# Kernel optimization log

Measured on AMD Instinct MI355X. Metric: run time of the kernel, lower is better.

## Reference

```python
import jax, jax.numpy as jnp
import numpy as np

EPI_AGE_PENALTY = 0.02
EPI_MIN_STRENGTH = 0.001
EPI_STRENGTH_BOOST = 0.5
RMS_EPS = 1e-6


def setup_inputs() -> dict:
    key = jax.random.key(0)
    k1, k2, k3, k4, k5, k6 = jax.random.split(key, 6)
    B, S, D = 32, 8192, 512
    return {
        "q_win": jax.random.normal(k1, (B, D), dtype=jnp.float32),
        "epi_keys": jax.random.normal(k2, (B, S, D), dtype=jnp.float32),
        "epi_vals": jax.random.normal(k3, (B, S, D), dtype=jnp.float32),
        "epi_age": jax.random.uniform(k4, (B, S), dtype=jnp.float32),
        "epi_strength": jax.random.uniform(k5, (B, S), dtype=jnp.float32),
        "scale": jnp.ones((D,), dtype=jnp.float32),  # RMSNorm learned scale
    }


def reference(q_win, epi_keys, epi_vals, epi_age, epi_strength, scale):
    # L2-normalize query [B,D] and keys [B,S,D]
    qn = q_win / (jnp.linalg.norm(q_win, axis=-1, keepdims=True) + 1e-6)
    kn = epi_keys / (jnp.linalg.norm(epi_keys, axis=-1, keepdims=True) + 1e-6)
    # cosine similarity [B,S]
    sim = jnp.einsum("bsd,bd->bs", kn, qn)
    str_log = jnp.log(jnp.clip(epi_strength, EPI_MIN_STRENGTH, 1e9))
    logits = sim + EPI_STRENGTH_BOOST * str_log - EPI_AGE_PENALTY * epi_age
    alive = (epi_strength > EPI_MIN_STRENGTH).astype(jnp.float32)
    logits = logits + (alive - 1.0) * 1000.0
    w = jax.nn.softmax(logits, axis=-1)
    # softmax-weighted read over slots -> [B,D]
    read = jnp.einsum("bs,bsd->bd", w, epi_vals)
    # RMSNorm
    rms = jnp.sqrt(jnp.mean(jnp.square(read), axis=-1, keepdims=True) + RMS_EPS)
    read = read / rms * scale
    return (read, w, logits)
```

## Files before the change

### kernel.cpp

```cpp
#include <hip/hip_runtime.h>
#include <math.h>

#define BB 32
#define SS 8192
#define DD 512
#define D4 (DD / 4)
#define CHUNKS 64
#define CHUNK 128

static constexpr float AGE_PEN = 0.02f;
static constexpr float MIN_STR = 0.001f;
static constexpr float STR_BOOST = 0.5f;
static constexpr float RMS_EPS_F = 1e-6f;

__device__ inline float dot4(float4 a, float4 b) {
    return a.x * b.x + a.y * b.y + a.z * b.z + a.w * b.w;
}

__device__ inline float block_sum(float v, volatile float* red) {
    int tid = threadIdx.x, lane = tid & 63, wid = tid >> 6;
#pragma unroll
    for (int off = 32; off; off >>= 1) v += __shfl_xor(v, off);
    if (lane == 0) red[wid] = v;
    __syncthreads();
    float r = red[0] + red[1] + red[2] + red[3];
    __syncthreads();
    return r;
}

__global__ __launch_bounds__(256) void fused_kernel(
    const float4* __restrict__ keys, const float4* __restrict__ vals,
    const float* __restrict__ q, const float* __restrict__ age,
    const float* __restrict__ strength, float* __restrict__ logits,
    float4* __restrict__ partial, float* __restrict__ esum_partial) {
    __shared__ float4 racc[4 * D4];
    __shared__ float e_sh[CHUNK];
    __shared__ float rede[4];

    int chunk = blockIdx.x, b = blockIdx.y;
    int tid = threadIdx.x, wid = tid >> 6, lane = tid & 63;

    const float4* q4 = (const float4*)q + b * D4;
    float4 q0 = q4[lane], q1 = q4[lane + 64];
    float qq = dot4(q0, q0) + dot4(q1, q1);
#pragma unroll
    for (int off = 32; off; off >>= 1) qq += __shfl_xor(qq, off);
    float qinv = 1.f / (sqrtf(qq) + 1e-6f);
    q0.x *= qinv; q0.y *= qinv; q0.z *= qinv; q0.w *= qinv;
    q1.x *= qinv; q1.y *= qinv; q1.z *= qinv; q1.w *= qinv;

    long long s0 = (long long)b * SS + chunk * CHUNK;

    float esum = 0.f;
#pragma unroll 2
    for (int s = wid; s < CHUNK; s += 4) {
        long long row = s0 + s;
        const float4* k = keys + row * D4;
        float4 k0 = k[lane], k1 = k[lane + 64];

        float kk = dot4(k0, k0) + dot4(k1, k1);
        float kq = dot4(k0, q0) + dot4(k1, q1);
#pragma unroll
        for (int off = 32; off; off >>= 1) {
            kk += __shfl_xor(kk, off);
            kq += __shfl_xor(kq, off);
        }
        float st = strength[row];
        float a = age[row];
        float lg = kq / (sqrtf(kk) + 1e-6f)
                 + STR_BOOST * logf(fminf(fmaxf(st, MIN_STR), 1e9f))
                 - AGE_PEN * a;
        if (!(st > MIN_STR)) lg -= 1000.f;
        float e = expf(lg);
        esum += e;
        if (lane == 0) {
            logits[row] = lg;
            e_sh[s] = e;
        }
    }
    if (lane == 0) rede[wid] = esum;
    __syncthreads();

    float4 acc0 = {0.f, 0.f, 0.f, 0.f}, acc1 = {0.f, 0.f, 0.f, 0.f};
#pragma unroll 4
    for (int s = wid; s < CHUNK; s += 4) {
        long long row = s0 + s;
        const float4* v = vals + row * D4;
        float e = e_sh[s];
        float4 v0 = v[lane], v1 = v[lane + 64];
        acc0.x += e * v0.x; acc0.y += e * v0.y; acc0.z += e * v0.z; acc0.w += e * v0.w;
        acc1.x += e * v1.x; acc1.y += e * v1.y; acc1.z += e * v1.z; acc1.w += e * v1.w;
    }

    racc[wid * D4 + lane] = acc0;
    racc[wid * D4 + 64 + lane] = acc1;
    __syncthreads();

    if (tid < D4) {
        float4 a0 = racc[tid], a1 = racc[D4 + tid], a2 = racc[2 * D4 + tid], a3 = racc[3 * D4 + tid];
        float4 r;
        r.x = a0.x + a1.x + a2.x + a3.x;
        r.y = a0.y + a1.y + a2.y + a3.y;
        r.z = a0.z + a1.z + a2.z + a3.z;
        r.w = a0.w + a1.w + a2.w + a3.w;
        partial[((long long)b * CHUNKS + chunk) * D4 + tid] = r;
    } else if (tid == D4) {
        esum_partial[b * CHUNKS + chunk] = rede[0] + rede[1] + rede[2] + rede[3];
    }
}

__global__ __launch_bounds__(256) void reduce_rms_kernel(
    const float* __restrict__ partial, const float* __restrict__ esum_partial,
    const float* __restrict__ scale, float* __restrict__ readout,
    float* __restrict__ inv_esum) {
    __shared__ float red[4];
    int b = blockIdx.x, tid = threadIdx.x;

    const float* p = partial + (long long)b * CHUNKS * DD;
    float r0 = 0.f, r1 = 0.f;
#pragma unroll 4
    for (int c = 0; c < CHUNKS; c++) {
        r0 += p[c * DD + tid];
        r1 += p[c * DD + tid + 256];
    }
    float le = (tid < CHUNKS) ? esum_partial[b * CHUNKS + tid] : 0.f;
    float etot = block_sum(le, red);
    float inv_e = 1.f / etot;
    if (tid == 0) inv_esum[b] = inv_e;
    r0 *= inv_e;
    r1 *= inv_e;
    float ss = block_sum(r0 * r0 + r1 * r1, red);
    float rms = sqrtf(ss / (float)DD + RMS_EPS_F);
    float inv = 1.f / rms;
    readout[b * DD + tid] = r0 * inv * scale[tid];
    readout[b * DD + tid + 256] = r1 * inv * scale[tid + 256];
}

__global__ __launch_bounds__(256) void w_kernel(const float4* __restrict__ logits,
                                                const float* __restrict__ inv_esum,
                                                float4* __restrict__ w) {
    int i4 = blockIdx.x * 256 + threadIdx.x;
    int b = i4 >> 11;
    float inv = inv_esum[b];
    float4 lg = logits[i4];
    float4 r;
    r.x = expf(lg.x) * inv;
    r.y = expf(lg.y) * inv;
    r.z = expf(lg.z) * inv;
    r.w = expf(lg.w) * inv;
    w[i4] = r;
}

extern "C" void kernel_launch(void* const* d_in, const int* in_sizes, int n_in,
                              void* d_out, int out_size, void* d_ws, size_t ws_size,
                              hipStream_t stream) {
    const float* q        = (const float*)d_in[0];
    const float* keys     = (const float*)d_in[1];
    const float* vals     = (const float*)d_in[2];
    const float* age      = (const float*)d_in[3];
    const float* strength = (const float*)d_in[4];
    const float* scale    = (const float*)d_in[5];

    float* out = (float*)d_out;
    float* readout = out;
    float* w       = out + BB * DD;
    float* logits  = out + BB * DD + BB * SS;

    float* ws = (float*)d_ws;
    float* partial      = ws;
    float* esum_partial = ws + BB * CHUNKS * DD;
    float* inv_esum     = esum_partial + BB * CHUNKS;

    fused_kernel<<<dim3(CHUNKS, BB), 256, 0, stream>>>(
        (const float4*)keys, (const float4*)vals, q, age, strength,
        logits, (float4*)partial, esum_partial);
    reduce_rms_kernel<<<BB, 256, 0, stream>>>(partial, esum_partial, scale, readout, inv_esum);
    w_kernel<<<BB * SS / 4 / 256, 256, 0, stream>>>((const float4*)logits, inv_esum, (float4*)w);
}
```

Measured before the change: 206.7 us.

## Split fused kernel into per-row logits kernel and separate weighted-sum kernel

```diff
diff --git a/kernel.cpp b/kernel.cpp
--- a/kernel.cpp
+++ b/kernel.cpp
@@ -28,17 +28,13 @@
     return r;
 }
 
-__global__ __launch_bounds__(256) void fused_kernel(
-    const float4* __restrict__ keys, const float4* __restrict__ vals,
-    const float* __restrict__ q, const float* __restrict__ age,
-    const float* __restrict__ strength, float* __restrict__ logits,
-    float4* __restrict__ partial, float* __restrict__ esum_partial) {
-    __shared__ float4 racc[4 * D4];
-    __shared__ float e_sh[CHUNK];
-    __shared__ float rede[4];
-
-    int chunk = blockIdx.x, b = blockIdx.y;
-    int tid = threadIdx.x, wid = tid >> 6, lane = tid & 63;
+__global__ __launch_bounds__(256) void logits_e_kernel(
+    const float4* __restrict__ keys, const float* __restrict__ q,
+    const float* __restrict__ age, const float* __restrict__ strength,
+    float* __restrict__ logits, float* __restrict__ e_out) {
+    int wid = threadIdx.x >> 6, lane = threadIdx.x & 63;
+    int row = blockIdx.x * 4 + wid;
+    int b = row >> 13;
 
     const float4* q4 = (const float4*)q + b * D4;
     float4 q0 = q4[lane], q1 = q4[lane + 64];
@@ -46,67 +42,57 @@
 #pragma unroll
     for (int off = 32; off; off >>= 1) qq += __shfl_xor(qq, off);
     float qinv = 1.f / (sqrtf(qq) + 1e-6f);
-    q0.x *= qinv; q0.y *= qinv; q0.z *= qinv; q0.w *= qinv;
-    q1.x *= qinv; q1.y *= qinv; q1.z *= qinv; q1.w *= qinv;
 
-    long long s0 = (long long)b * SS + chunk * CHUNK;
-
-    float esum = 0.f;
-#pragma unroll 2
-    for (int s = wid; s < CHUNK; s += 4) {
-        long long row = s0 + s;
-        const float4* k = keys + row * D4;
-        float4 k0 = k[lane], k1 = k[lane + 64];
-
-        float kk = dot4(k0, k0) + dot4(k1, k1);
-        float kq = dot4(k0, q0) + dot4(k1, q1);
+    const float4* k = keys + (long long)row * D4;
+    float4 k0 = k[lane], k1 = k[lane + 64];
+    float kk = dot4(k0, k0) + dot4(k1, k1);
+    float kq = dot4(k0, q0) + dot4(k1, q1);
 #pragma unroll
-        for (int off = 32; off; off >>= 1) {
-            kk += __shfl_xor(kk, off);
-            kq += __shfl_xor(kq, off);
-        }
+    for (int off = 32; off; off >>= 1) {
+        kk += __shfl_xor(kk, off);
+        kq += __shfl_xor(kq, off);
+    }
+    if (lane == 0) {
         float st = strength[row];
         float a = age[row];
-        float lg = kq / (sqrtf(kk) + 1e-6f)
-                 + STR_BOOST * logf(fminf(fmaxf(st, MIN_STR), 1e9f))
-                 - AGE_PEN * a;
+        float sim = kq * qinv / (sqrtf(kk) + 1e-6f);
+        float lg = sim + STR_BOOST * logf(fminf(fmaxf(st, MIN_STR), 1e9f)) - AGE_PEN * a;
         if (!(st > MIN_STR)) lg -= 1000.f;
-        float e = expf(lg);
-        esum += e;
-        if (lane == 0) {
-            logits[row] = lg;
-            e_sh[s] = e;
-        }
+        logits[row] = lg;
+        e_out[row] = expf(lg);
     }
-    if (lane == 0) rede[wid] = esum;
+}
+
+__global__ __launch_bounds__(128) void wsum_kernel(
+    const float4* __restrict__ vals, const float* __restrict__ e,
+    float4* __restrict__ partial, float* __restrict__ esum_partial) {
+    __shared__ float sw[CHUNK];
+    __shared__ float rede[2];
+    int chunk = blockIdx.x, b = blockIdx.y, tid = threadIdx.x;
+    int s0 = chunk * CHUNK;
+    float my_e = e[b * SS + s0 + tid];
+    sw[tid] = my_e;
     __syncthreads();
 
-    float4 acc0 = {0.f, 0.f, 0.f, 0.f}, acc1 = {0.f, 0.f, 0.f, 0.f};
+    const float4* vbase = vals + ((long long)b * SS + s0) * D4 + tid;
+    float4 acc = {0.f, 0.f, 0.f, 0.f};
 #pragma unroll 4
-    for (int s = wid; s < CHUNK; s += 4) {
-        long long row = s0 + s;
-        const float4* v = vals + row * D4;
-        float e = e_sh[s];
-        float4 v0 = v[lane], v1 = v[lane + 64];
-        acc0.x += e * v0.x; acc0.y += e * v0.y; acc0.z += e * v0.z; acc0.w += e * v0.w;
-        acc1.x += e * v1.x; acc1.y += e * v1.y; acc1.z += e * v1.z; acc1.w += e * v1.w;
+    for (int s = 0; s < CHUNK; s++) {
+        float4 v = vbase[(long long)s * D4];
+        float ww = sw[s];
+        acc.x += ww * v.x;
+        acc.y += ww * v.y;
+        acc.z += ww * v.z;
+        acc.w += ww * v.w;
     }
+    partial[((long long)b * CHUNKS + chunk) * D4 + tid] = acc;
 
-    racc[wid * D4 + lane] = acc0;
-    racc[wid * D4 + 64 + lane] = acc1;
+    float t = my_e;
+#pragma unroll
+    for (int off = 32; off; off >>= 1) t += __shfl_xor(t, off);
+    if ((tid & 63) == 0) rede[tid >> 6] = t;
     __syncthreads();
-
-    if (tid < D4) {
-        float4 a0 = racc[tid], a1 = racc[D4 + tid], a2 = racc[2 * D4 + tid], a3 = racc[3 * D4 + tid];
-        float4 r;
-        r.x = a0.x + a1.x + a2.x + a3.x;
-        r.y = a0.y + a1.y + a2.y + a3.y;
-        r.z = a0.z + a1.z + a2.z + a3.z;
-        r.w = a0.w + a1.w + a2.w + a3.w;
-        partial[((long long)b * CHUNKS + chunk) * D4 + tid] = r;
-    } else if (tid == D4) {
-        esum_partial[b * CHUNKS + chunk] = rede[0] + rede[1] + rede[2] + rede[3];
-    }
+    if (tid == 0) esum_partial[b * CHUNKS + chunk] = rede[0] + rede[1];
 }
 
 __global__ __launch_bounds__(256) void reduce_rms_kernel(
@@ -136,19 +122,14 @@
     readout[b * DD + tid + 256] = r1 * inv * scale[tid + 256];
 }
 
-__global__ __launch_bounds__(256) void w_kernel(const float4* __restrict__ logits,
-                                                const float* __restrict__ inv_esum,
-                                                float4* __restrict__ w) {
+__global__ __launch_bounds__(256) void w_scale_kernel(float4* __restrict__ w,
+                                                      const float* __restrict__ inv_esum) {
     int i4 = blockIdx.x * 256 + threadIdx.x;
     int b = i4 >> 11;
     float inv = inv_esum[b];
-    float4 lg = logits[i4];
-    float4 r;
-    r.x = expf(lg.x) * inv;
-    r.y = expf(lg.y) * inv;
-    r.z = expf(lg.z) * inv;
-    r.w = expf(lg.w) * inv;
-    w[i4] = r;
+    float4 v = w[i4];
+    v.x *= inv; v.y *= inv; v.z *= inv; v.w *= inv;
+    w[i4] = v;
 }
 
 extern "C" void kernel_launch(void* const* d_in, const int* in_sizes, int n_in,
@@ -171,9 +152,10 @@
     float* esum_partial = ws + BB * CHUNKS * DD;
     float* inv_esum     = esum_partial + BB * CHUNKS;
 
-    fused_kernel<<<dim3(CHUNKS, BB), 256, 0, stream>>>(
-        (const float4*)keys, (const float4*)vals, q, age, strength,
-        logits, (float4*)partial, esum_partial);
+    logits_e_kernel<<<BB * SS / 4, 256, 0, stream>>>(
+        (const float4*)keys, q, age, strength, logits, w);
+    wsum_kernel<<<dim3(CHUNKS, BB), 128, 0, stream>>>(
+        (const float4*)vals, w, (float4*)partial, esum_partial);
     reduce_rms_kernel<<<BB, 256, 0, stream>>>(partial, esum_partial, scale, readout, inv_esum);
-    w_kernel<<<BB * SS / 4 / 256, 256, 0, stream>>>((const float4*)logits, inv_esum, (float4*)w);
+    w_scale_kernel<<<BB * SS / 4 / 256, 256, 0, stream>>>((float4*)w, inv_esum);
 }
```

Result: faster. 201.7 us (-2.4%).
